# Optimization experiments

Measured on AMD Instinct MI355X. Metric: run time of the kernel, lower is better.

The kernel has to match this reference:

```python
import jax, jax.numpy as jnp
import numpy as np

jax.config.update("jax_enable_x64", True)  # original uses double for Cholesky stability

LAM = 1.0


def _safe_pow(x, a):
    # |x|**a, with a gradient-safe handling of x == 0 (result is 0 for a > 0;
    # naive 0**a has nan grad w.r.t. a via log(0)).
    ax = jnp.abs(x)
    safe = jnp.where(ax == 0, 1.0, ax)
    return jnp.where(ax == 0, 0.0, safe ** a)


def _dx_cov(alpha, tau, T):
    # fGn (increment) covariance; stationary -> depends only on lag k = j - i (Toeplitz)
    t = jnp.arange(T - 1, dtype=jnp.float64)
    DT = (t[None, :] - t[:, None])[None, :, :]          # [1, T-1, T-1]
    a = alpha[:, None, None].astype(jnp.float64)        # [BS, 1, 1]
    tb = tau[:, None, None].astype(jnp.float64)
    R = 0.5 * (_safe_pow(DT + 1.0, a) + _safe_pow(DT - 1.0, a) - 2.0 * _safe_pow(DT, a))
    adt = jnp.abs(DT)
    # exponential taper beyond lag tau; clamp exponent so unused branch can't overflow
    decay = jnp.exp(-LAM * jnp.maximum(adt - tb, 0.0))
    R = jnp.where(adt >= tb, R * decay, R)
    return R                                            # [BS, T-1, T-1] float64


def setup_inputs() -> dict:
    key = jax.random.key(0)
    k1, k2, k3, k4 = jax.random.split(key, 4)
    BS, T, dim = 64, 1024, 3
    alpha = (0.5 + jax.random.uniform(k1, (BS,))).astype(jnp.float32)        # (0.5, 1.5) valid fBM exponent
    tau = (20.0 + 50.0 * jax.random.uniform(k2, (BS,))).astype(jnp.float32)  # taper lag > 0
    diffusion = (0.5 + jax.random.uniform(k3, (BS,))).astype(jnp.float32)
    du = jax.random.normal(k4, (BS, T - 1, dim), dtype=jnp.float32)          # hoisted torch.randn
    return {"alpha": alpha, "tau": tau, "diffusion": diffusion, "du": du, "T": T}


def reference(alpha, tau, diffusion, du, T):
    BS, dim = alpha.shape[0], du.shape[-1]
    C = _dx_cov(alpha, tau, T)                           # [BS, T-1, T-1] float64
    L = jnp.linalg.cholesky(C).astype(jnp.float32)       # batched Cholesky, cast like torch
    du_s = du * jnp.sqrt(diffusion)[:, None, None]       # scale noise by sqrt(D)
    dx = L @ du_s                                        # [BS, T-1, dim]
    x = jnp.cumsum(dx, axis=1)
    zeros = jnp.zeros((BS, 1, dim), dtype=x.dtype)
    return jnp.concatenate([zeros, x], axis=1)           # [BS, T, dim]
```

## Files before the change

kernel.cpp:

```cpp
#include <hip/hip_runtime.h>
#include <math.h>


#define TM1 1023
#define NTH 256
#define K0  128

__device__ __forceinline__ float bperm(int a, float v) {
    return __int_as_float(__builtin_amdgcn_ds_bpermute(a, __float_as_int(v)));
}
__device__ __forceinline__ float rdlane(float v, int s) {
    return __int_as_float(__builtin_amdgcn_readlane(__float_as_int(v), s));
}
__device__ __forceinline__ int uslot(int k) { return ((k & 3) << 8) | (k >> 2); }

__global__ __launch_bounds__(NTH, 1)
void fbm_schur_kernel(const float* __restrict__ alpha,
                      const float* __restrict__ tau,
                      const float* __restrict__ diffusion,
                      const float* __restrict__ du,
                      float* __restrict__ out)
{
    const int b   = blockIdx.x;
    const int tid = threadIdx.x;
    const int w   = tid >> 6;
    const int l   = tid & 63;

    __shared__ float  colD[K0 * 128];
    __shared__ float4 us4[1024];
    __shared__ float  yx[1024], yy[1024], yz[1024];
    __shared__ float  Lc[128];
    __shared__ float  wtot[12];

    const float sd = sqrtf(diffusion[b]);
    const float* dub = du + (size_t)b * (TM1 * 3);

    for (int e = tid; e < TM1 * 3; e += NTH) {
        int k = e / 3, d = e - 3 * k;
        ((float*)&us4[uslot(k)])[d] = dub[e] * sd;
    }
    for (int i = tid; i < 1024; i += NTH) { yx[i] = 0.f; yy[i] = 0.f; yz[i] = 0.f; }

    float g1a = 0.f, g1b = 0.f, g2a = 0.f, g2b = 0.f;
    if (w == 0) {
        const double a  = (double)alpha[b];
        const double tb = (double)tau[b];
        auto cov = [&](int k) -> float {
            if (k == 0) return 1.0f;
            double dk = (double)k;
            double ck = 0.5 * (pow(dk + 1.0, a) + pow(dk - 1.0, a) - 2.0 * pow(dk, a));
            if (dk >= tb) ck *= exp(tb - dk);
            return (float)ck;
        };
        g1a = cov(l);
        g1b = cov(l + 64);
        g2a = (l == 0) ? 0.f : g1a;
        g2b = g1b;
    }
    __syncthreads();

    if (w == 0) {
        const int addr_up = ((l + 1) & 63) << 2;
        for (int k = 0; k < K0; ++k) {
            colD[k * 128 + l]      = g1a;
            colD[k * 128 + 64 + l] = g1b;
            float den  = rdlane(g1a, 0);
            float num  = rdlane(g2a, 1);
            float r    = num * __builtin_amdgcn_rcpf(den);
            float wrap = rdlane(g2b, 0);
            float g2pa = bperm(addr_up, g2a);
            float g2pb = bperm(addr_up, g2b);
            if (l == 63) { g2pa = wrap; g2pb = 0.f; }
            float n1a = fmaf(-r, g2pa, g1a);
            float n1b = fmaf(-r, g2pb, g1b);
            g2a = fmaf(-r, g1a, g2pa);
            g2b = fmaf(-r, g1b, g2pb);
            g1a = n1a; g1b = n1b;
        }
        float sc = __frsqrt_rn(rdlane(g1a, 0));
        Lc[l]      = g1a * sc;
        Lc[64 + l] = g1b * sc;
    }
    __syncthreads();

    {
        float4 v0 = us4[uslot(l)];
        float4 v1 = us4[uslot(64 + l)];
        float i0 = __frsqrt_rn(colD[l * 128]);
        float i1 = __frsqrt_rn(colD[(64 + l) * 128]);
        float ucx0 = v0.x * i0, ucy0 = v0.y * i0, ucz0 = v0.z * i0;
        float ucx1 = v1.x * i1, ucy1 = v1.y * i1, ucz1 = v1.z * i1;

        float ax = 0.f, ay = 0.f, az = 0.f;
        #pragma unroll 4
        for (int k2 = 0; k2 < 64; ++k2) {
            int p = tid - k2;
            float v = colD[k2 * 128 + p];
            v = ((unsigned)p < 128u) ? v : 0.f;
            ax = fmaf(v, rdlane(ucx0, k2), ax);
            ay = fmaf(v, rdlane(ucy0, k2), ay);
            az = fmaf(v, rdlane(ucz0, k2), az);
        }
        #pragma unroll 4
        for (int k2 = 64; k2 < 128; ++k2) {
            int p = tid - k2;
            float v = colD[k2 * 128 + p];
            v = ((unsigned)p < 128u) ? v : 0.f;
            ax = fmaf(v, rdlane(ucx1, k2 - 64), ax);
            ay = fmaf(v, rdlane(ucy1, k2 - 64), ay);
            az = fmaf(v, rdlane(ucz1, k2 - 64), az);
        }
        yx[tid] = ax; yy[tid] = ay; yz[tid] = az;
    }
    __syncthreads();

    {
        float lca = Lc[l], lcb = Lc[64 + l];
        const int B = K0 + 4 * tid;
        float4 q0 = us4[uslot(B + 0)];
        float4 q1 = us4[uslot(B + 1)];
        float4 q2 = us4[uslot(B + 2)];
        float4 q3 = us4[uslot(B + 3)];
        float a0x=0,a0y=0,a0z=0, a1x=0,a1y=0,a1z=0;
        float a2x=0,a2y=0,a2z=0, a3x=0,a3y=0,a3z=0;

        #pragma unroll 8
        for (int j = 0; j < 64; ++j) {
            float lc = rdlane(lca, j);
            a0x = fmaf(lc, q0.x, a0x); a0y = fmaf(lc, q0.y, a0y); a0z = fmaf(lc, q0.z, a0z);
            a1x = fmaf(lc, q1.x, a1x); a1y = fmaf(lc, q1.y, a1y); a1z = fmaf(lc, q1.z, a1z);
            a2x = fmaf(lc, q2.x, a2x); a2y = fmaf(lc, q2.y, a2y); a2z = fmaf(lc, q2.z, a2z);
            a3x = fmaf(lc, q3.x, a3x); a3y = fmaf(lc, q3.y, a3y); a3z = fmaf(lc, q3.z, a3z);
            int xi = B - j - 1;
            float4 nv = us4[uslot(xi)];
            bool ok = (xi >= K0);
            nv.x = ok ? nv.x : 0.f; nv.y = ok ? nv.y : 0.f; nv.z = ok ? nv.z : 0.f;
            q3 = q2; q2 = q1; q1 = q0; q0 = nv;
        }
        #pragma unroll 8
        for (int j = 64; j < 128; ++j) {
            float lc = rdlane(lcb, j - 64);
            a0x = fmaf(lc, q0.x, a0x); a0y = fmaf(lc, q0.y, a0y); a0z = fmaf(lc, q0.z, a0z);
            a1x = fmaf(lc, q1.x, a1x); a1y = fmaf(lc, q1.y, a1y); a1z = fmaf(lc, q1.z, a1z);
            a2x = fmaf(lc, q2.x, a2x); a2y = fmaf(lc, q2.y, a2y); a2z = fmaf(lc, q2.z, a2z);
            a3x = fmaf(lc, q3.x, a3x); a3y = fmaf(lc, q3.y, a3y); a3z = fmaf(lc, q3.z, a3z);
            int xi = B - j - 1;
            float4 nv = us4[uslot(xi)];
            bool ok = (xi >= K0);
            nv.x = ok ? nv.x : 0.f; nv.y = ok ? nv.y : 0.f; nv.z = ok ? nv.z : 0.f;
            q3 = q2; q2 = q1; q1 = q0; q0 = nv;
        }
        if (B + 0 <= 1022) { yx[B+0] += a0x; yy[B+0] += a0y; yz[B+0] += a0z; }
        if (B + 1 <= 1022) { yx[B+1] += a1x; yy[B+1] += a1y; yz[B+1] += a1z; }
        if (B + 2 <= 1022) { yx[B+2] += a2x; yy[B+2] += a2y; yz[B+2] += a2z; }
        if (B + 3 <= 1022) { yx[B+3] += a3x; yy[B+3] += a3y; yz[B+3] += a3z; }
    }
    __syncthreads();

    float cx = 0.f, cy = 0.f, cz = 0.f;
    for (int s = 0; s < 4; ++s) {
        int i = (w << 8) + (s << 6) + l;
        float sx = (i < TM1) ? yx[i] : 0.f;
        float sy = (i < TM1) ? yy[i] : 0.f;
        float sz = (i < TM1) ? yz[i] : 0.f;
        #pragma unroll
        for (int off = 1; off < 64; off <<= 1) {
            float tx = __shfl_up(sx, off);
            float ty = __shfl_up(sy, off);
            float tz = __shfl_up(sz, off);
            if (l >= off) { sx += tx; sy += ty; sz += tz; }
        }
        sx += cx; sy += cy; sz += cz;
        if (i < TM1) { yx[i] = sx; yy[i] = sy; yz[i] = sz; }
        cx = __shfl(sx, 63); cy = __shfl(sy, 63); cz = __shfl(sz, 63);
    }
    if (l == 0) { wtot[w * 3 + 0] = cx; wtot[w * 3 + 1] = cy; wtot[w * 3 + 2] = cz; }
    __syncthreads();

    float ox = 0.f, oy = 0.f, oz = 0.f;
    for (int q = 0; q < w; ++q) {
        ox += wtot[q * 3 + 0]; oy += wtot[q * 3 + 1]; oz += wtot[q * 3 + 2];
    }
    float* outb = out + (size_t)b * (TM1 + 1) * 3;
    for (int s = 0; s < 4; ++s) {
        int i = (w << 8) + (s << 6) + l;
        if (i < TM1) {
            outb[(i + 1) * 3 + 0] = yx[i] + ox;
            outb[(i + 1) * 3 + 1] = yy[i] + oy;
            outb[(i + 1) * 3 + 2] = yz[i] + oz;
        }
    }
    if (tid == 0) { outb[0] = 0.f; outb[1] = 0.f; outb[2] = 0.f; }
}

extern "C" void kernel_launch(void* const* d_in, const int* in_sizes, int n_in,
                              void* d_out, int out_size, void* d_ws, size_t ws_size,
                              hipStream_t stream)
{
    const float* alpha     = (const float*)d_in[0];
    const float* tau       = (const float*)d_in[1];
    const float* diffusion = (const float*)d_in[2];
    const float* du        = (const float*)d_in[3];
    float* out = (float*)d_out;
    const int BS = in_sizes[0];

    fbm_schur_kernel<<<dim3(BS), dim3(NTH), 0, stream>>>(
        alpha, tau, diffusion, du, out);
}
```

Before: 87.21 us.

## Use float asymptotic covariance and two-step fused Schur recursion

Replaces the double-precision pow/exp covariance with float powf for small lags and a series expansion of the second difference for large lags, removing slow FP64 transcendental calls. The Schur generator recursion now advances two steps per iteration, so the reflection coefficients for both steps are computed from the current generators and the serial dependency chain of cross-lane shuffles is halved. This risks accuracy loss from float arithmetic and the truncated series, and the two-step recurrence may be less numerically stable than the single-step form.

Measured after the change: 87.96 us, median of 2. Within noise of the previous version (+0.9%).

```diff
diff --git a/kernel.cpp b/kernel.cpp
--- a/kernel.cpp
+++ b/kernel.cpp
@@ -43,39 +43,77 @@
 
     float g1a = 0.f, g1b = 0.f, g2a = 0.f, g2b = 0.f;
     if (w == 0) {
-        const double a  = (double)alpha[b];
-        const double tb = (double)tau[b];
-        auto cov = [&](int k) -> float {
+        const float af = alpha[b];
+        const float tf = tau[b];
+        const float c2 = (af - 2.f) * (af - 3.f) * (1.f / 12.f);
+        const float c3 = (af - 2.f) * (af - 3.f) * (af - 4.f) * (af - 5.f) * (1.f / 360.f);
+        const float lead = 0.5f * af * (af - 1.f);
+        auto covf = [&](int k) -> float {
             if (k == 0) return 1.0f;
-            double dk = (double)k;
-            double ck = 0.5 * (pow(dk + 1.0, a) + pow(dk - 1.0, a) - 2.0 * pow(dk, a));
-            if (dk >= tb) ck *= exp(tb - dk);
-            return (float)ck;
+            float kf = (float)k;
+            float R;
+            if (k < 8) {
+                float pm = (k == 1) ? 0.f : powf(kf - 1.f, af);
+                R = 0.5f * (powf(kf + 1.f, af) + pm - 2.f * powf(kf, af));
+            } else {
+                float x2 = 1.f / (kf * kf);
+                float poly = 1.f + x2 * (c2 + x2 * c3);
+                float kp = exp2f((af - 2.f) * log2f(kf));
+                R = lead * kp * poly;
+            }
+            if (kf >= tf) R *= exp2f((tf - kf) * 1.44269504f);
+            return R;
         };
-        g1a = cov(l);
-        g1b = cov(l + 64);
+        g1a = covf(l);
+        g1b = covf(l + 64);
         g2a = (l == 0) ? 0.f : g1a;
         g2b = g1b;
     }
     __syncthreads();
 
     if (w == 0) {
-        const int addr_up = ((l + 1) & 63) << 2;
-        for (int k = 0; k < K0; ++k) {
-            colD[k * 128 + l]      = g1a;
-            colD[k * 128 + 64 + l] = g1b;
-            float den  = rdlane(g1a, 0);
-            float num  = rdlane(g2a, 1);
-            float r    = num * __builtin_amdgcn_rcpf(den);
-            float wrap = rdlane(g2b, 0);
-            float g2pa = bperm(addr_up, g2a);
-            float g2pb = bperm(addr_up, g2b);
-            if (l == 63) { g2pa = wrap; g2pb = 0.f; }
-            float n1a = fmaf(-r, g2pa, g1a);
-            float n1b = fmaf(-r, g2pb, g1b);
-            g2a = fmaf(-r, g1a, g2pa);
-            g2b = fmaf(-r, g1b, g2pb);
+        const int ad1 = ((l + 1) & 63) << 2;
+        const int ad2 = ((l + 2) & 63) << 2;
+        for (int k = 0; k < K0; k += 2) {
+            float g1a1 = bperm(ad1, g1a);
+            float g1b1 = bperm(ad1, g1b);
+            float g2a1 = bperm(ad1, g2a);
+            float g2b1 = bperm(ad1, g2b);
+            float g2a2 = bperm(ad2, g2a);
+            float g2b2 = bperm(ad2, g2b);
+
+            float s10 = rdlane(g1a, 0);
+            float s11 = rdlane(g1a, 1);
+            float s21 = rdlane(g2a, 1);
+            float s22 = rdlane(g2a, 2);
+            float r1  = s21 * __builtin_amdgcn_rcpf(s10);
+            float r2  = fmaf(s10, s22, -s21 * s11) *
+                        __builtin_amdgcn_rcpf(fmaf(s10, s10, -s21 * s21));
+            float r12 = r1 * r2;
+
+            float wg1b0 = rdlane(g1b, 0);
+            float wg2b0 = rdlane(g2b, 0);
+            float wg2b1 = rdlane(g2b, 1);
+            if (l == 62) { g2a2 = wg2b0; g2b2 = 0.f; }
+            if (l == 63) {
+                g1a1 = wg1b0; g1b1 = 0.f;
+                g2a1 = wg2b0; g2b1 = 0.f;
+                g2a2 = wg2b1; g2b2 = 0.f;
+            }
+
+            float c1a = fmaf(-r1, g2a1, g1a);
+            float c1b = fmaf(-r1, g2b1, g1b);
+            colD[k * 128 + l]            = g1a;
+            colD[k * 128 + 64 + l]       = g1b;
+            colD[(k + 1) * 128 + l]      = c1a;
+            colD[(k + 1) * 128 + 64 + l] = c1b;
+
+            float n1a = fmaf(r12, g1a1, fmaf(-r2, g2a2, c1a));
+            float n1b = fmaf(r12, g1b1, fmaf(-r2, g2b2, c1b));
+            float n2a = fmaf(r12, g2a1, fmaf(-r1, g1a1, fmaf(-r2, g1a, g2a2)));
+            float n2b = fmaf(r12, g2b1, fmaf(-r1, g1b1, fmaf(-r2, g1b, g2b2)));
             g1a = n1a; g1b = n1b;
+            g2a = n2a; g2b = n2b;
         }
         float sc = __frsqrt_rn(rdlane(g1a, 0));
         Lc[l]      = g1a * sc;
```
